# Optimization experiments

Hardware: AMD Instinct MI355X
Metric: run time of the kernel (lower is better)

## Reference

```python
import jax, jax.numpy as jnp
import numpy as np

U, V, A = 100000, 50000, 5000   # n_users, n_videos, n_vloggers
D = 64                           # latent_dim_rec
N_LAYERS = 3                     # VAGNN_n_layers
NNZ_UI, NNZ_UA, NNZ_G2, NNZ_G4 = 4_000_000, 2_000_000, 200_000, 2_000_000
BATCH = 1024

def spmm(rows, cols, vals, x, n_rows):
    # sparse.mm(COO(rows, cols, vals), x) -> [n_rows, d]
    return jax.ops.segment_sum(vals[:, None] * x[cols], rows, num_segments=n_rows)

def one_propagate(rows, cols, vals, a_feat, b_feat):
    # LightGCN propagation: mean over layer-0..n embeddings (running sum, no stack)
    n = a_feat.shape[0] + b_feat.shape[0]
    feats = jnp.concatenate([a_feat, b_feat], axis=0)
    acc, cur = feats, feats
    for _ in range(N_LAYERS):
        cur = spmm(rows, cols, vals, cur, n)
        acc = acc + cur
    light = acc / (N_LAYERS + 1)
    return light[:a_feat.shape[0]], light[a_feat.shape[0]:]

def l2norm(x):
    # F.normalize(x, dim=1), eps=1e-12
    return x / jnp.maximum(jnp.linalg.norm(x, axis=1, keepdims=True), 1e-12)

def setup_inputs() -> dict:
    key = jax.random.key(0)
    ks = jax.random.split(key, 16)
    return {
        'emb_user':    jax.random.normal(ks[0], (U, D), jnp.float32) * 0.1,
        'emb_video':   jax.random.normal(ks[1], (V, D), jnp.float32) * 0.1,
        'emb_vlogger': jax.random.normal(ks[2], (A, D), jnp.float32) * 0.1,
        'q':           jax.random.normal(ks[3], (D, D), jnp.float32) * 0.1,
        'ui_rows': jax.random.randint(ks[4], (NNZ_UI,), 0, U + V, jnp.int32),
        'ui_cols': jax.random.randint(ks[5], (NNZ_UI,), 0, U + V, jnp.int32),
        'ui_vals': jax.random.uniform(ks[6], (NNZ_UI,), jnp.float32) * 0.01,
        'ua_rows': jax.random.randint(ks[7], (NNZ_UA,), 0, U + A, jnp.int32),
        'ua_cols': jax.random.randint(ks[8], (NNZ_UA,), 0, U + A, jnp.int32),
        'ua_vals': jax.random.uniform(ks[9], (NNZ_UA,), jnp.float32) * 0.01,
        'g2_rows': jax.random.randint(ks[10], (NNZ_G2,), 0, A, jnp.int32),
        'g2_cols': jax.random.randint(ks[11], (NNZ_G2,), 0, V, jnp.int32),
        'g2_vals': jax.random.uniform(ks[12], (NNZ_G2,), jnp.float32) * 0.01,
        'g4_rows': jax.random.randint(ks[13], (NNZ_G4,), 0, V, jnp.int32),
        'g4_cols': jax.random.randint(ks[14], (NNZ_G4,), 0, U, jnp.int32),
        'g4_vals': jax.random.uniform(ks[15], (NNZ_G4,), jnp.float32) * 0.01,
        'vlogger_list': jax.random.randint(jax.random.fold_in(key, 100), (V,), 0, A, jnp.int32),
        'users': jax.random.randint(jax.random.fold_in(key, 101), (BATCH,), 0, U, jnp.int32),
    }

def reference(emb_user, emb_video, emb_vlogger, q,
              ui_rows, ui_cols, ui_vals,
              ua_rows, ua_cols, ua_vals,
              g2_rows, g2_cols, g2_vals,
              g4_rows, g4_cols, g4_vals,
              vlogger_list, users):
    # computer()
    atom_u, atom_v = one_propagate(ui_rows, ui_cols, ui_vals, emb_user, emb_video)
    atom_a = l2norm(spmm(g2_rows, g2_cols, g2_vals, atom_v, A))
    non_u, non_a = one_propagate(ua_rows, ua_cols, ua_vals, emb_user, emb_vlogger)
    non_v = l2norm(spmm(g4_rows, g4_cols, g4_vals, non_u, V))
    # getUsersRating()
    u_a, u_n = atom_u[users], non_u[users]                 # [B, D]
    vl_a, vl_n = atom_a[vlogger_list], non_a[vlogger_list]  # [V, D]
    ui = jax.nn.sigmoid(u_a @ atom_v.T + u_n @ non_v.T)      # [B, V]
    ua = jax.nn.sigmoid(u_a @ vl_a.T + u_n @ vl_n.T)         # [B, V]
    vid = (atom_v + non_v) * 0.5
    vlog = (vl_a + vl_n) * 0.5
    w = jax.nn.sigmoid(jnp.sum((vid @ q) * vlog, axis=1))    # [V]
    return w * ui + (1.0 - w) * ua
```

## Files before the change

### kernel.cpp

```cpp
#include <hip/hip_runtime.h>
#include <hip/hip_bf16.h>

#define U_N 100000
#define V_N 50000
#define A_N 5000

typedef float4 f4;
typedef unsigned int u32;
typedef __attribute__((ext_vector_type(8))) short bf16x8;
typedef __attribute__((ext_vector_type(4))) float f32x4;

__device__ inline float bflo(u32 p) { return __uint_as_float(p << 16); }
__device__ inline float bfhi(u32 p) { return __uint_as_float(p & 0xffff0000u); }
__device__ inline u32 f2bf(float f) {
  u32 u = __float_as_uint(f);
  return (u + 0x7fffu + ((u >> 16) & 1u)) >> 16;
}
__device__ inline u32 pack2(float lo, float hi) {
  return f2bf(lo) | (f2bf(hi) << 16);
}
__device__ inline bf16x8 ld8(const u32* p) {
  uint4 u = *(const uint4*)p;
  return __builtin_bit_cast(bf16x8, u);
}

__global__ void k_concat2b(const float* __restrict__ a, int na,
                           const float* __restrict__ b, int nb,
                           u32* __restrict__ curH, float* __restrict__ acc) {
  int total4 = (na + nb) * 16;
  for (int i = blockIdx.x * blockDim.x + threadIdx.x; i < total4;
       i += gridDim.x * blockDim.x) {
    int fi = i * 4;
    f4 v = (fi < na * 64) ? *(const f4*)(a + fi)
                          : *(const f4*)(b + (fi - na * 64));
    *(f4*)(acc + fi) = v;
    uint2 h; h.x = pack2(v.x, v.y); h.y = pack2(v.z, v.w);
    *(uint2*)(curH + (fi >> 1)) = h;
  }
}

__global__ void k_count(const int* __restrict__ rows, int nnz, int* __restrict__ cnt) {
  for (int i = blockIdx.x * blockDim.x + threadIdx.x; i < nnz;
       i += gridDim.x * blockDim.x)
    atomicAdd(&cnt[rows[i]], 1);
}

__global__ void k_bsum(const int* __restrict__ cnt, int n, int* __restrict__ bsum) {
  __shared__ int red[1024];
  int t = threadIdx.x;
  int i = blockIdx.x * 1024 + t;
  red[t] = (i < n) ? cnt[i] : 0;
  __syncthreads();
  for (int off = 512; off; off >>= 1) {
    if (t < off) red[t] += red[t + off];
    __syncthreads();
  }
  if (t == 0) bsum[blockIdx.x] = red[0];
}

__global__ void k_bscan(int* __restrict__ bsum, int nb) {
  if (threadIdx.x == 0) {
    int run = 0;
    for (int i = 0; i < nb; ++i) {
      int c = bsum[i];
      bsum[i] = run;
      run += c;
    }
  }
}

__global__ void k_bapply(const int* __restrict__ cnt, int n,
                         const int* __restrict__ bsum,
                         int* __restrict__ rp, int* __restrict__ pos) {
  __shared__ int sc[1024];
  int t = threadIdx.x;
  int i = blockIdx.x * 1024 + t;
  int c = (i < n) ? cnt[i] : 0;
  sc[t] = c;
  __syncthreads();
  #pragma unroll
  for (int off = 1; off < 1024; off <<= 1) {
    int v = (t >= off) ? sc[t - off] : 0;
    __syncthreads();
    sc[t] += v;
    __syncthreads();
  }
  int val = bsum[blockIdx.x] + sc[t] - c;
  if (i < n) {
    rp[i] = val;
    pos[i] = val;
    if (i == n - 1) rp[n] = val + c;
  }
}

__global__ void k_fill(const int* __restrict__ rows, const int* __restrict__ cols,
                       const float* __restrict__ vals, int nnz,
                       int* __restrict__ pos, int2* __restrict__ ep) {
  for (int i = blockIdx.x * blockDim.x + threadIdx.x; i < nnz;
       i += gridDim.x * blockDim.x) {
    int slot = atomicAdd(&pos[rows[i]], 1);
    ep[slot] = make_int2(cols[i], __float_as_int(vals[i]));
  }
}

__global__ void k_mark(const int* __restrict__ users, int nb,
                       int* __restrict__ flag, int* __restrict__ rcount,
                       int* __restrict__ rlist) {
  int b = blockIdx.x * blockDim.x + threadIdx.x;
  if (b < nb) {
    int u = users[b];
    if (atomicExch(&flag[u], 1) == 0) {
      int m = atomicAdd(rcount, 1);
      rlist[m] = u;
    }
  }
}

__device__ __forceinline__ void spmm_row(
    int row, const int* __restrict__ rp, const int2* __restrict__ ep,
    const u32* __restrict__ inH, int instrU,
    u32* __restrict__ outH, int ostrU, int ocolU,
    float* __restrict__ acc, int l2n, int wout, int lane, int eg, int du) {
  int e0 = rp[row], e1 = rp[row + 1];
  float s[8] = {0.f, 0.f, 0.f, 0.f, 0.f, 0.f, 0.f, 0.f};
  int e = e0 + eg;
  for (; e + 8 < e1; e += 16) {
    int2 ed0 = ep[e];
    int2 ed1 = ep[e + 8];
    float v0 = __int_as_float(ed0.y), v1 = __int_as_float(ed1.y);
    uint4 x0 = *(const uint4*)(inH + (size_t)ed0.x * instrU + du);
    uint4 x1 = *(const uint4*)(inH + (size_t)ed1.x * instrU + du);
    s[0] = fmaf(v0, bflo(x0.x), s[0]); s[1] = fmaf(v0, bfhi(x0.x), s[1]);
    s[2] = fmaf(v0, bflo(x0.y), s[2]); s[3] = fmaf(v0, bfhi(x0.y), s[3]);
    s[4] = fmaf(v0, bflo(x0.z), s[4]); s[5] = fmaf(v0, bfhi(x0.z), s[5]);
    s[6] = fmaf(v0, bflo(x0.w), s[6]); s[7] = fmaf(v0, bfhi(x0.w), s[7]);
    s[0] = fmaf(v1, bflo(x1.x), s[0]); s[1] = fmaf(v1, bfhi(x1.x), s[1]);
    s[2] = fmaf(v1, bflo(x1.y), s[2]); s[3] = fmaf(v1, bfhi(x1.y), s[3]);
    s[4] = fmaf(v1, bflo(x1.z), s[4]); s[5] = fmaf(v1, bfhi(x1.z), s[5]);
    s[6] = fmaf(v1, bflo(x1.w), s[6]); s[7] = fmaf(v1, bfhi(x1.w), s[7]);
  }
  if (e < e1) {
    int2 ed0 = ep[e];
    float v0 = __int_as_float(ed0.y);
    uint4 x0 = *(const uint4*)(inH + (size_t)ed0.x * instrU + du);
    s[0] = fmaf(v0, bflo(x0.x), s[0]); s[1] = fmaf(v0, bfhi(x0.x), s[1]);
    s[2] = fmaf(v0, bflo(x0.y), s[2]); s[3] = fmaf(v0, bfhi(x0.y), s[3]);
    s[4] = fmaf(v0, bflo(x0.z), s[4]); s[5] = fmaf(v0, bfhi(x0.z), s[5]);
    s[6] = fmaf(v0, bflo(x0.w), s[6]); s[7] = fmaf(v0, bfhi(x0.w), s[7]);
  }
  #pragma unroll
  for (int j = 0; j < 8; ++j) {
    s[j] += __shfl_xor(s[j], 8);
    s[j] += __shfl_xor(s[j], 16);
    s[j] += __shfl_xor(s[j], 32);
  }
  if (l2n) {
    float ss = 0.f;
    #pragma unroll
    for (int j = 0; j < 8; ++j) ss = fmaf(s[j], s[j], ss);
    ss += __shfl_xor(ss, 1);
    ss += __shfl_xor(ss, 2);
    ss += __shfl_xor(ss, 4);
    float inv = 1.0f / fmaxf(sqrtf(ss), 1e-12f);
    #pragma unroll
    for (int j = 0; j < 8; ++j) s[j] *= inv;
  }
  if (eg == 0) {
    if (wout) {
      uint4 o;
      o.x = pack2(s[0], s[1]); o.y = pack2(s[2], s[3]);
      o.z = pack2(s[4], s[5]); o.w = pack2(s[6], s[7]);
      *(uint4*)(outH + (size_t)row * ostrU + ocolU + du) = o;
    }
    if (acc) {
      float* ap = acc + (size_t)row * 64 + (lane & 7) * 8;
      f4 a0 = *(f4*)ap, a1 = *(f4*)(ap + 4);
      a0.x += s[0]; a0.y += s[1]; a0.z += s[2]; a0.w += s[3];
      a1.x += s[4]; a1.y += s[5]; a1.z += s[6]; a1.w += s[7];
      *(f4*)ap = a0; *(f4*)(ap + 4) = a1;
    }
  }
}

__global__ void k_spmm_b(const int* __restrict__ rp, const int2* __restrict__ ep,
                         int nrows, int rbase,
                         const u32* __restrict__ inH, int instrU,
                         u32* __restrict__ outH, int ostrU, int ocolU,
                         float* __restrict__ acc, int l2n, int wout) {
  int lane = threadIdx.x & 63;
  int w = (blockIdx.x * blockDim.x + threadIdx.x) >> 6;
  int nw = (gridDim.x * blockDim.x) >> 6;
  int eg = lane >> 3;
  int du = (lane & 7) * 4;
  for (int r = w; r < nrows; r += nw)
    spmm_row(rbase + r, rp, ep, inH, instrU, outH, ostrU, ocolU, acc, l2n, wout,
             lane, eg, du);
}

__global__ void k_spmm_b_list(const int* __restrict__ rp, const int2* __restrict__ ep,
                              const int* __restrict__ rlist, const int* __restrict__ rcount,
                              const u32* __restrict__ inH, int instrU,
                              float* __restrict__ acc) {
  int lane = threadIdx.x & 63;
  int w = (blockIdx.x * blockDim.x + threadIdx.x) >> 6;
  int nw = (gridDim.x * blockDim.x) >> 6;
  int eg = lane >> 3;
  int du = (lane & 7) * 4;
  int m = *rcount;
  for (int r = w; r < m; r += nw)
    spmm_row(rlist[r], rp, ep, inH, instrU, nullptr, 0, 0, acc, 0, 0,
             lane, eg, du);
}

__global__ void k_scale_ua(float* __restrict__ acc, u32* __restrict__ UAuH) {
  int total4 = (U_N + A_N) * 16;
  for (int i = blockIdx.x * blockDim.x + threadIdx.x; i < total4;
       i += gridDim.x * blockDim.x) {
    int fi = i * 4;
    f4 v = *(f4*)(acc + fi);
    v.x *= 0.25f; v.y *= 0.25f; v.z *= 0.25f; v.w *= 0.25f;
    *(f4*)(acc + fi) = v;
    if (fi < U_N * 64) {
      uint2 h; h.x = pack2(v.x, v.y); h.y = pack2(v.z, v.w);
      *(uint2*)(UAuH + (fi >> 1)) = h;
    }
  }
}

__global__ void k_scale_ui(float* __restrict__ acc, u32* __restrict__ VAH) {
  int total4 = (U_N + V_N) * 16;
  for (int i = blockIdx.x * blockDim.x + threadIdx.x; i < total4;
       i += gridDim.x * blockDim.x) {
    int fi = i * 4;
    f4 v = *(f4*)(acc + fi);
    v.x *= 0.25f; v.y *= 0.25f; v.z *= 0.25f; v.w *= 0.25f;
    *(f4*)(acc + fi) = v;
    if (fi >= U_N * 64) {
      int rem = fi - U_N * 64;
      int row = rem >> 6, col = rem & 63;
      uint2 h; h.x = pack2(v.x, v.y); h.y = pack2(v.z, v.w);
      *(uint2*)(VAH + (size_t)row * 64 + (col >> 1)) = h;
    }
  }
}

__global__ void k_gather_u(const int* __restrict__ users,
                           const float* __restrict__ accUI,
                           const float* __restrict__ accUA,
                           u32* __restrict__ UcatH) {
  int b = blockIdx.x;
  int t = threadIdx.x;
  int u = users[b];
  UcatH[b * 64 + t] = pack2(accUI[(size_t)u * 64 + 2 * t], accUI[(size_t)u * 64 + 2 * t + 1]);
  UcatH[b * 64 + 32 + t] = pack2(accUA[(size_t)u * 64 + 2 * t], accUA[(size_t)u * 64 + 2 * t + 1]);
}

__global__ void k_gather_vb(const int* __restrict__ vlist,
                            const u32* __restrict__ atomAH,
                            const float* __restrict__ accUA,
                            u32* __restrict__ VBH) {
  int v = blockIdx.x * 4 + (threadIdx.x >> 5);
  int t = threadIdx.x & 31;
  int a = vlist[v];
  VBH[(size_t)v * 64 + t] = atomAH[(size_t)a * 32 + t];
  VBH[(size_t)v * 64 + 32 + t] =
      pack2(accUA[(size_t)(U_N + a) * 64 + 2 * t], accUA[(size_t)(U_N + a) * 64 + 2 * t + 1]);
}

__global__ void k_w(const u32* __restrict__ VAH, const u32* __restrict__ VBH,
                    const float* __restrict__ q, float* __restrict__ wv) {
  __shared__ float qs[64 * 64];
  for (int i = threadIdx.x; i < 4096; i += blockDim.x) qs[i] = q[i];
  __syncthreads();
  int lane = threadIdx.x & 63;
  int v = blockIdx.x * 4 + (threadIdx.x >> 6);
  if (v >= V_N) return;
  int half = lane & 1;
  u32 pa0 = VAH[(size_t)v * 64 + (lane >> 1)];
  u32 pa1 = VAH[(size_t)v * 64 + 32 + (lane >> 1)];
  u32 pb0 = VBH[(size_t)v * 64 + (lane >> 1)];
  u32 pb1 = VBH[(size_t)v * 64 + 32 + (lane >> 1)];
  float vid = 0.5f * ((half ? bfhi(pa0) : bflo(pa0)) + (half ? bfhi(pa1) : bflo(pa1)));
  float vlog = 0.5f * ((half ? bfhi(pb0) : bflo(pb0)) + (half ? bfhi(pb1) : bflo(pb1)));
  float s = 0.0f;
  for (int d = 0; d < 64; ++d)
    s = fmaf(__shfl(vid, d, 64), qs[d * 64 + lane], s);
  float t = s * vlog;
  #pragma unroll
  for (int off = 32; off; off >>= 1) t += __shfl_xor(t, off, 64);
  if (lane == 0) wv[v] = 1.0f / (1.0f + __expf(-t));
}

__global__ __launch_bounds__(256) void k_rating_mfma(
    const u32* __restrict__ UcatH, const u32* __restrict__ VAH,
    const u32* __restrict__ VBH, const float* __restrict__ wv,
    float* __restrict__ out) {
  int lane = threadIdx.x & 63;
  int wave = threadIdx.x >> 6;
  int n0 = blockIdx.x * 64;
  int m0 = blockIdx.y * 256 + wave * 64;
  int rr = lane & 15, g = lane >> 4;
  f32x4 accA[4][4], accB[4][4];
  #pragma unroll
  for (int i = 0; i < 4; ++i)
    #pragma unroll
    for (int j = 0; j < 4; ++j) {
      accA[i][j] = (f32x4){0.f, 0.f, 0.f, 0.f};
      accB[i][j] = (f32x4){0.f, 0.f, 0.f, 0.f};
    }
  #pragma unroll
  for (int ks = 0; ks < 4; ++ks) {
    int ko = ks * 16 + g * 4;
    bf16x8 a[4], bA[4], bB[4];
    #pragma unroll
    for (int i = 0; i < 4; ++i)
      a[i] = ld8(UcatH + (size_t)(m0 + i * 16 + rr) * 64 + ko);
    #pragma unroll
    for (int j = 0; j < 4; ++j) {
      int nr = n0 + j * 16 + rr;
      if (nr >= V_N) nr = V_N - 1;
      bA[j] = ld8(VAH + (size_t)nr * 64 + ko);
      bB[j] = ld8(VBH + (size_t)nr * 64 + ko);
    }
    #pragma unroll
    for (int i = 0; i < 4; ++i)
      #pragma unroll
      for (int j = 0; j < 4; ++j) {
        accA[i][j] = __builtin_amdgcn_mfma_f32_16x16x32_bf16(a[i], bA[j], accA[i][j], 0, 0, 0);
        accB[i][j] = __builtin_amdgcn_mfma_f32_16x16x32_bf16(a[i], bB[j], accB[i][j], 0, 0, 0);
      }
  }
  #pragma unroll
  for (int j = 0; j < 4; ++j) {
    int v = n0 + j * 16 + rr;
    if (v >= V_N) continue;
    float wvv = wv[v];
    #pragma unroll
    for (int i = 0; i < 4; ++i) {
      #pragma unroll
      for (int reg = 0; reg < 4; ++reg) {
        int u = m0 + i * 16 + g * 4 + reg;
        float sa = 1.0f / (1.0f + __expf(-accA[i][j][reg]));
        float sb = 1.0f / (1.0f + __expf(-accB[i][j][reg]));
        out[(size_t)u * V_N + v] = wvv * sa + (1.0f - wvv) * sb;
      }
    }
  }
}

extern "C" void kernel_launch(void* const* d_in, const int* in_sizes, int n_in,
                              void* d_out, int out_size, void* d_ws, size_t ws_size,
                              hipStream_t stream) {
  const float* emb_user    = (const float*)d_in[0];
  const float* emb_video   = (const float*)d_in[1];
  const float* emb_vlogger = (const float*)d_in[2];
  const float* q           = (const float*)d_in[3];
  const int*   ui_rows = (const int*)d_in[4];
  const int*   ui_cols = (const int*)d_in[5];
  const float* ui_vals = (const float*)d_in[6];
  const int*   ua_rows = (const int*)d_in[7];
  const int*   ua_cols = (const int*)d_in[8];
  const float* ua_vals = (const float*)d_in[9];
  const int*   g2_rows = (const int*)d_in[10];
  const int*   g2_cols = (const int*)d_in[11];
  const float* g2_vals = (const float*)d_in[12];
  const int*   g4_rows = (const int*)d_in[13];
  const int*   g4_cols = (const int*)d_in[14];
  const float* g4_vals = (const float*)d_in[15];
  const int*   vlist   = (const int*)d_in[16];
  const int*   users   = (const int*)d_in[17];
  int nnz_ui = in_sizes[4], nnz_ua = in_sizes[7];
  int nnz_g2 = in_sizes[10], nnz_g4 = in_sizes[13];

  float* ws = (float*)d_ws;
  float* accUI = ws;
  float* accUA = ws + 9600000;
  u32*   curH  = (u32*)(ws + 16320000);
  u32*   nxtH  = (u32*)(ws + 21120000);
  u32*   VAH   = (u32*)(ws + 25920000);
  u32*   VBH   = (u32*)(ws + 29120000);
  u32*   UAuH  = (u32*)(ws + 32320000);
  u32*   UcatH = (u32*)(ws + 35520000);
  u32*   atomAH= (u32*)(ws + 35585536);
  float* wv    = ws + 35745536;
  int*   bsum  = (int*)(ws + 35795536);
  int*   ib    = (int*)(ws + 35800000);
  int*   flag   = (int*)VBH;
  int*   rcount = flag + 100000;
  int*   rlist  = flag + 100016;

  const int nUI = U_N + V_N, nUA = U_N + A_N;
  auto nr_pad = [](int nrows) { return (size_t)((nrows + 1 + 15) & ~15); };

  auto build_csr = [&](const int* rows, const int* cols, const float* vals,
                       int nnz, int nrows, int* rp, int* pos, int2* ep) {
    hipMemsetAsync(pos, 0, (size_t)nrows * 4, stream);
    k_count<<<2048, 256, 0, stream>>>(rows, nnz, pos);
    int nb = (nrows + 1023) / 1024;
    k_bsum<<<nb, 1024, 0, stream>>>(pos, nrows, bsum);
    k_bscan<<<1, 64, 0, stream>>>(bsum, nb);
    k_bapply<<<nb, 1024, 0, stream>>>(pos, nrows, bsum, rp, pos);
    k_fill<<<2048, 256, 0, stream>>>(rows, cols, vals, nnz, pos, ep);
  };

  {
    size_t NR = nr_pad(nUI);
    int* rp = ib; int* pos = ib + NR; int2* ep = (int2*)(ib + 2 * NR);
    build_csr(ui_rows, ui_cols, ui_vals, nnz_ui, nUI, rp, pos, ep);
    k_concat2b<<<2048, 256, 0, stream>>>(emb_user, U_N, emb_video, V_N, curH, accUI);
    hipMemsetAsync(flag, 0, (size_t)(100016) * 4, stream);
    k_mark<<<4, 256, 0, stream>>>(users, 1024, flag, rcount, rlist);
    k_spmm_b<<<2048, 256, 0, stream>>>(rp, ep, nUI, 0, curH, 32, nxtH, 32, 0, accUI, 0, 1);
    k_spmm_b<<<2048, 256, 0, stream>>>(rp, ep, nUI, 0, nxtH, 32, curH, 32, 0, accUI, 0, 1);
    k_spmm_b<<<2048, 256, 0, stream>>>(rp, ep, V_N, U_N, curH, 32, nullptr, 0, 0, accUI, 0, 0);
    k_spmm_b_list<<<16, 256, 0, stream>>>(rp, ep, rlist, rcount, curH, 32, accUI);
  }
  {
    size_t NR = nr_pad(nUA);
    int* rp = ib; int* pos = ib + NR; int2* ep = (int2*)(ib + 2 * NR);
    build_csr(ua_rows, ua_cols, ua_vals, nnz_ua, nUA, rp, pos, ep);
    k_concat2b<<<2048, 256, 0, stream>>>(emb_user, U_N, emb_vlogger, A_N, curH, accUA);
    k_spmm_b<<<2048, 256, 0, stream>>>(rp, ep, nUA, 0, curH, 32, nxtH, 32, 0, accUA, 0, 1);
    k_spmm_b<<<2048, 256, 0, stream>>>(rp, ep, nUA, 0, nxtH, 32, curH, 32, 0, accUA, 0, 1);
    k_spmm_b<<<2048, 256, 0, stream>>>(rp, ep, nUA, 0, curH, 32, nullptr, 0, 0, accUA, 0, 0);
  }
  k_scale_ua<<<2048, 256, 0, stream>>>(accUA, UAuH);
  k_scale_ui<<<2048, 256, 0, stream>>>(accUI, VAH);
  size_t NR4 = nr_pad(V_N), NR2 = nr_pad(A_N);
  int* rp4 = ib; int* pos4 = ib + NR4; int2* ep4 = (int2*)(ib + 2 * NR4);
  int* ib2 = (int*)(ep4 + nnz_g4);
  int* rp2 = ib2; int* pos2 = ib2 + NR2; int2* ep2 = (int2*)(ib2 + 2 * NR2);
  build_csr(g4_rows, g4_cols, g4_vals, nnz_g4, V_N, rp4, pos4, ep4);
  build_csr(g2_rows, g2_cols, g2_vals, nnz_g2, A_N, rp2, pos2, ep2);
  k_spmm_b<<<2048, 256, 0, stream>>>(rp2, ep2, A_N, 0, VAH, 64, atomAH, 32, 0, nullptr, 1, 1);
  k_spmm_b<<<2048, 256, 0, stream>>>(rp4, ep4, V_N, 0, UAuH, 32, VAH, 64, 32, nullptr, 1, 1);
  k_gather_u<<<1024, 32, 0, stream>>>(users, accUI, accUA, UcatH);
  k_gather_vb<<<12500, 128, 0, stream>>>(vlist, atomAH, accUA, VBH);
  k_w<<<12500, 256, 0, stream>>>(VAH, VBH, q, wv);
  dim3 gridR((V_N + 63) / 64, 1024 / 256);
  k_rating_mfma<<<gridR, 256, 0, stream>>>(UcatH, VAH, VBH, wv, (float*)d_out);
}
```

Before: 1.720 ms.

## Build CSR via two-pass row-bucket binning to localize scatter writes

Replaces the single-pass atomic scatter of COO entries into CSR with a two-stage scheme. Entries are first binned into 128-row buckets in a staging buffer that reuses the accumulator and current-feature workspace, then each bucket is flushed by one block into its final slots, so the final scatter stays within a small, cache-resident range. It also raises the grid of the listed-row SpMM kernel from 16 to 256 blocks. The cost is an extra pass and 16-byte staging writes, and correctness depends on the staging aliases not overlapping data that is still live.

```diff
diff --git a/kernel.cpp b/kernel.cpp
--- a/kernel.cpp
+++ b/kernel.cpp
@@ -4,6 +4,8 @@
 #define U_N 100000
 #define V_N 50000
 #define A_N 5000
+#define RPB 128
+#define RPB_SH 7
 
 typedef float4 f4;
 typedef unsigned int u32;
@@ -100,6 +102,35 @@
        i += gridDim.x * blockDim.x) {
     int slot = atomicAdd(&pos[rows[i]], 1);
     ep[slot] = make_int2(cols[i], __float_as_int(vals[i]));
+  }
+}
+
+__global__ void k_seed(const int* __restrict__ rp, int nbkt, int* __restrict__ bcur) {
+  int b = blockIdx.x * blockDim.x + threadIdx.x;
+  if (b < nbkt) bcur[b] = rp[b << RPB_SH];
+}
+
+__global__ void k_binfill(const int* __restrict__ rows, const int* __restrict__ cols,
+                          const float* __restrict__ vals, int nnz,
+                          int* __restrict__ bcur, int4* __restrict__ stg) {
+  for (int i = blockIdx.x * blockDim.x + threadIdx.x; i < nnz;
+       i += gridDim.x * blockDim.x) {
+    int r = rows[i];
+    int idx = atomicAdd(&bcur[r >> RPB_SH], 1);
+    stg[idx] = make_int4(r, cols[i], __float_as_int(vals[i]), 0);
+  }
+}
+
+__global__ void k_bflush(const int4* __restrict__ stg, const int* __restrict__ rp,
+                         int nrows, int* __restrict__ pos, int2* __restrict__ ep) {
+  int b = blockIdx.x;
+  int r0 = b << RPB_SH;
+  int r1 = min(r0 + RPB, nrows);
+  int start = rp[r0], end = rp[r1];
+  for (int idx = start + threadIdx.x; idx < end; idx += blockDim.x) {
+    int4 e = stg[idx];
+    int slot = atomicAdd(&pos[e.x], 1);
+    ep[slot] = make_int2(e.y, e.z);
   }
 }
 
@@ -384,7 +415,10 @@
   u32*   atomAH= (u32*)(ws + 35585536);
   float* wv    = ws + 35745536;
   int*   bsum  = (int*)(ws + 35795536);
+  int*   bcur  = (int*)(ws + 35795800);
   int*   ib    = (int*)(ws + 35800000);
+  int4*  stgUI = (int4*)accUI;
+  int4*  stgCN = (int4*)curH;
   int*   flag   = (int*)VBH;
   int*   rcount = flag + 100000;
   int*   rlist  = flag + 100016;
@@ -392,33 +426,47 @@
   const int nUI = U_N + V_N, nUA = U_N + A_N;
   auto nr_pad = [](int nrows) { return (size_t)((nrows + 1 + 15) & ~15); };
 
-  auto build_csr = [&](const int* rows, const int* cols, const float* vals,
-                       int nnz, int nrows, int* rp, int* pos, int2* ep) {
+  auto build_rp = [&](const int* rows, int nnz, int nrows, int* rp, int* pos) {
     hipMemsetAsync(pos, 0, (size_t)nrows * 4, stream);
     k_count<<<2048, 256, 0, stream>>>(rows, nnz, pos);
     int nb = (nrows + 1023) / 1024;
     k_bsum<<<nb, 1024, 0, stream>>>(pos, nrows, bsum);
     k_bscan<<<1, 64, 0, stream>>>(bsum, nb);
     k_bapply<<<nb, 1024, 0, stream>>>(pos, nrows, bsum, rp, pos);
+  };
+
+  auto build_csr_binned = [&](const int* rows, const int* cols, const float* vals,
+                              int nnz, int nrows, int* rp, int* pos, int2* ep,
+                              int4* stg) {
+    build_rp(rows, nnz, nrows, rp, pos);
+    int nbkt = (nrows + RPB - 1) >> RPB_SH;
+    k_seed<<<(nbkt + 255) / 256, 256, 0, stream>>>(rp, nbkt, bcur);
+    k_binfill<<<2048, 256, 0, stream>>>(rows, cols, vals, nnz, bcur, stg);
+    k_bflush<<<nbkt, 256, 0, stream>>>(stg, rp, nrows, pos, ep);
+  };
+
+  auto build_csr_simple = [&](const int* rows, const int* cols, const float* vals,
+                              int nnz, int nrows, int* rp, int* pos, int2* ep) {
+    build_rp(rows, nnz, nrows, rp, pos);
     k_fill<<<2048, 256, 0, stream>>>(rows, cols, vals, nnz, pos, ep);
   };
 
   {
     size_t NR = nr_pad(nUI);
     int* rp = ib; int* pos = ib + NR; int2* ep = (int2*)(ib + 2 * NR);
-    build_csr(ui_rows, ui_cols, ui_vals, nnz_ui, nUI, rp, pos, ep);
+    build_csr_binned(ui_rows, ui_cols, ui_vals, nnz_ui, nUI, rp, pos, ep, stgUI);
     k_concat2b<<<2048, 256, 0, stream>>>(emb_user, U_N, emb_video, V_N, curH, accUI);
     hipMemsetAsync(flag, 0, (size_t)(100016) * 4, stream);
     k_mark<<<4, 256, 0, stream>>>(users, 1024, flag, rcount, rlist);
     k_spmm_b<<<2048, 256, 0, stream>>>(rp, ep, nUI, 0, curH, 32, nxtH, 32, 0, accUI, 0, 1);
     k_spmm_b<<<2048, 256, 0, stream>>>(rp, ep, nUI, 0, nxtH, 32, curH, 32, 0, accUI, 0, 1);
     k_spmm_b<<<2048, 256, 0, stream>>>(rp, ep, V_N, U_N, curH, 32, nullptr, 0, 0, accUI, 0, 0);
-    k_spmm_b_list<<<16, 256, 0, stream>>>(rp, ep, rlist, rcount, curH, 32, accUI);
+    k_spmm_b_list<<<256, 256, 0, stream>>>(rp, ep, rlist, rcount, curH, 32, accUI);
   }
   {
     size_t NR = nr_pad(nUA);
     int* rp = ib; int* pos = ib + NR; int2* ep = (int2*)(ib + 2 * NR);
-    build_csr(ua_rows, ua_cols, ua_vals, nnz_ua, nUA, rp, pos, ep);
+    build_csr_binned(ua_rows, ua_cols, ua_vals, nnz_ua, nUA, rp, pos, ep, stgCN);
     k_concat2b<<<2048, 256, 0, stream>>>(emb_user, U_N, emb_vlogger, A_N, curH, accUA);
     k_spmm_b<<<2048, 256, 0, stream>>>(rp, ep, nUA, 0, curH, 32, nxtH, 32, 0, accUA, 0, 1);
     k_spmm_b<<<2048, 256, 0, stream>>>(rp, ep, nUA, 0, nxtH, 32, curH, 32, 0, accUA, 0, 1);
@@ -430,8 +478,8 @@
   int* rp4 = ib; int* pos4 = ib + NR4; int2* ep4 = (int2*)(ib + 2 * NR4);
   int* ib2 = (int*)(ep4 + nnz_g4);
   int* rp2 = ib2; int* pos2 = ib2 + NR2; int2* ep2 = (int2*)(ib2 + 2 * NR2);
-  build_csr(g4_rows, g4_cols, g4_vals, nnz_g4, V_N, rp4, pos4, ep4);
-  build_csr(g2_rows, g2_cols, g2_vals, nnz_g2, A_N, rp2, pos2, ep2);
+  build_csr_binned(g4_rows, g4_cols, g4_vals, nnz_g4, V_N, rp4, pos4, ep4, stgCN);
+  build_csr_simple(g2_rows, g2_cols, g2_vals, nnz_g2, A_N, rp2, pos2, ep2);
   k_spmm_b<<<2048, 256, 0, stream>>>(rp2, ep2, A_N, 0, VAH, 64, atomAH, 32, 0, nullptr, 1, 1);
   k_spmm_b<<<2048, 256, 0, stream>>>(rp4, ep4, V_N, 0, UAuH, 32, VAH, 64, 32, nullptr, 1, 1);
   k_gather_u<<<1024, 32, 0, stream>>>(users, accUI, accUA, UcatH);
```

Result: slower. 3.151 ms (+83.1%).

## Window CSR build count/fill passes by row range for atomic and write locality

Applied to the files above, without the earlier changes.

The CSR count and fill passes are split into several launches, each handling only the rows inside a fixed window (16384 or 8192 rows). Each launch's atomics and edge-pair writes then land in a smaller region of memory, which should cut cache thrashing from scattered accesses. In exchange, every pass re-reads the full rows array once per window (about ten passes for UI), which adds read bandwidth and launch overhead. The grid of the user-list SpMM kernel is also raised from 16 to 256 blocks to spread that work across more CUs.

```diff
diff --git a/kernel.cpp b/kernel.cpp
--- a/kernel.cpp
+++ b/kernel.cpp
@@ -39,10 +39,13 @@
   }
 }
 
-__global__ void k_count(const int* __restrict__ rows, int nnz, int* __restrict__ cnt) {
+__global__ void k_count(const int* __restrict__ rows, int nnz,
+                        int* __restrict__ cnt, int r0, int r1) {
   for (int i = blockIdx.x * blockDim.x + threadIdx.x; i < nnz;
-       i += gridDim.x * blockDim.x)
-    atomicAdd(&cnt[rows[i]], 1);
+       i += gridDim.x * blockDim.x) {
+    int r = rows[i];
+    if (r >= r0 && r < r1) atomicAdd(&cnt[r], 1);
+  }
 }
 
 __global__ void k_bsum(const int* __restrict__ cnt, int n, int* __restrict__ bsum) {
@@ -95,11 +98,15 @@
 
 __global__ void k_fill(const int* __restrict__ rows, const int* __restrict__ cols,
                        const float* __restrict__ vals, int nnz,
-                       int* __restrict__ pos, int2* __restrict__ ep) {
+                       int* __restrict__ pos, int2* __restrict__ ep,
+                       int r0, int r1) {
   for (int i = blockIdx.x * blockDim.x + threadIdx.x; i < nnz;
        i += gridDim.x * blockDim.x) {
-    int slot = atomicAdd(&pos[rows[i]], 1);
-    ep[slot] = make_int2(cols[i], __float_as_int(vals[i]));
+    int r = rows[i];
+    if (r >= r0 && r < r1) {
+      int slot = atomicAdd(&pos[r], 1);
+      ep[slot] = make_int2(cols[i], __float_as_int(vals[i]));
+    }
   }
 }
 
@@ -393,32 +400,35 @@
   auto nr_pad = [](int nrows) { return (size_t)((nrows + 1 + 15) & ~15); };
 
   auto build_csr = [&](const int* rows, const int* cols, const float* vals,
-                       int nnz, int nrows, int* rp, int* pos, int2* ep) {
+                       int nnz, int nrows, int win, int* rp, int* pos, int2* ep) {
     hipMemsetAsync(pos, 0, (size_t)nrows * 4, stream);
-    k_count<<<2048, 256, 0, stream>>>(rows, nnz, pos);
+    for (int r0 = 0; r0 < nrows; r0 += win)
+      k_count<<<2048, 256, 0, stream>>>(rows, nnz, pos, r0, min(r0 + win, nrows));
     int nb = (nrows + 1023) / 1024;
     k_bsum<<<nb, 1024, 0, stream>>>(pos, nrows, bsum);
     k_bscan<<<1, 64, 0, stream>>>(bsum, nb);
     k_bapply<<<nb, 1024, 0, stream>>>(pos, nrows, bsum, rp, pos);
-    k_fill<<<2048, 256, 0, stream>>>(rows, cols, vals, nnz, pos, ep);
+    for (int r0 = 0; r0 < nrows; r0 += win)
+      k_fill<<<2048, 256, 0, stream>>>(rows, cols, vals, nnz, pos, ep,
+                                       r0, min(r0 + win, nrows));
   };
 
   {
     size_t NR = nr_pad(nUI);
     int* rp = ib; int* pos = ib + NR; int2* ep = (int2*)(ib + 2 * NR);
-    build_csr(ui_rows, ui_cols, ui_vals, nnz_ui, nUI, rp, pos, ep);
+    build_csr(ui_rows, ui_cols, ui_vals, nnz_ui, nUI, 16384, rp, pos, ep);
     k_concat2b<<<2048, 256, 0, stream>>>(emb_user, U_N, emb_video, V_N, curH, accUI);
     hipMemsetAsync(flag, 0, (size_t)(100016) * 4, stream);
     k_mark<<<4, 256, 0, stream>>>(users, 1024, flag, rcount, rlist);
     k_spmm_b<<<2048, 256, 0, stream>>>(rp, ep, nUI, 0, curH, 32, nxtH, 32, 0, accUI, 0, 1);
     k_spmm_b<<<2048, 256, 0, stream>>>(rp, ep, nUI, 0, nxtH, 32, curH, 32, 0, accUI, 0, 1);
     k_spmm_b<<<2048, 256, 0, stream>>>(rp, ep, V_N, U_N, curH, 32, nullptr, 0, 0, accUI, 0, 0);
-    k_spmm_b_list<<<16, 256, 0, stream>>>(rp, ep, rlist, rcount, curH, 32, accUI);
+    k_spmm_b_list<<<256, 256, 0, stream>>>(rp, ep, rlist, rcount, curH, 32, accUI);
   }
   {
     size_t NR = nr_pad(nUA);
     int* rp = ib; int* pos = ib + NR; int2* ep = (int2*)(ib + 2 * NR);
-    build_csr(ua_rows, ua_cols, ua_vals, nnz_ua, nUA, rp, pos, ep);
+    build_csr(ua_rows, ua_cols, ua_vals, nnz_ua, nUA, 16384, rp, pos, ep);
     k_concat2b<<<2048, 256, 0, stream>>>(emb_user, U_N, emb_vlogger, A_N, curH, accUA);
     k_spmm_b<<<2048, 256, 0, stream>>>(rp, ep, nUA, 0, curH, 32, nxtH, 32, 0, accUA, 0, 1);
     k_spmm_b<<<2048, 256, 0, stream>>>(rp, ep, nUA, 0, nxtH, 32, curH, 32, 0, accUA, 0, 1);
@@ -430,8 +440,8 @@
   int* rp4 = ib; int* pos4 = ib + NR4; int2* ep4 = (int2*)(ib + 2 * NR4);
   int* ib2 = (int*)(ep4 + nnz_g4);
   int* rp2 = ib2; int* pos2 = ib2 + NR2; int2* ep2 = (int2*)(ib2 + 2 * NR2);
-  build_csr(g4_rows, g4_cols, g4_vals, nnz_g4, V_N, rp4, pos4, ep4);
-  build_csr(g2_rows, g2_cols, g2_vals, nnz_g2, A_N, rp2, pos2, ep2);
+  build_csr(g4_rows, g4_cols, g4_vals, nnz_g4, V_N, 8192, rp4, pos4, ep4);
+  build_csr(g2_rows, g2_cols, g2_vals, nnz_g2, A_N, 8192, rp2, pos2, ep2);
   k_spmm_b<<<2048, 256, 0, stream>>>(rp2, ep2, A_N, 0, VAH, 64, atomAH, 32, 0, nullptr, 1, 1);
   k_spmm_b<<<2048, 256, 0, stream>>>(rp4, ep4, V_N, 0, UAuH, 32, VAH, 64, 32, nullptr, 1, 1);
   k_gather_u<<<1024, 32, 0, stream>>>(users, accUI, accUA, UcatH);
```

Measured after the change: 1.796 ms. 1.04x slower.
